# Kernel optimization log

Measured on AMD Instinct MI355X. Metric: run time of the kernel, lower is better.

## Reference

```python
import jax, jax.numpy as jnp
import numpy as np

N = 8192          # number of atoms
N_ELEM = 95       # r2r4 table size (elements 0..94)
EPS = 1e-12


def setup_inputs() -> dict:
    key = jax.random.key(0)
    k1, k2, k3 = jax.random.split(key, 3)
    atomic_numbers = jax.random.randint(k1, (N,), 0, N_ELEM)
    # positions in a ~60 Angstrom box so pair distances are realistic
    positions = jax.random.uniform(k2, (N, 3), dtype=jnp.float32) * 60.0
    r2r4 = jax.random.uniform(k3, (N_ELEM,), dtype=jnp.float32)
    # Becke-Johnson damping parameters (PBE D3-BJ)
    a1 = jnp.float32(0.4289)
    a2 = jnp.float32(4.4407)
    s6 = jnp.float32(1.0)
    s8 = jnp.float32(0.7875)
    return {"atomic_numbers": atomic_numbers, "positions": positions,
            "r2r4": r2r4, "a1": a1, "a2": a2, "s6": s6, "s8": s8}


def reference(atomic_numbers, positions, r2r4, a1, a2, s6, s8):
    # Per-atom-type gather (present in source; mathematically unused because
    # the source hard-codes c6 = c8 = 1 via all-ones LazyTensors).
    r2r4_z = r2r4[atomic_numbers]                      # (N,)

    # All-pairs squared distances. d appears only as d^6 and d^8, which are
    # polynomials in d2, so no sqrt is needed (also keeps diagonal smooth).
    diff = positions[:, None, :] - positions[None, :, :]   # (N, N, 3)
    d2 = jnp.sum(diff * diff, axis=-1)                     # (N, N)
    d6 = d2 * d2 * d2
    d8 = d6 * d2

    # c6 = c8 = 1  =>  tmp = a1 * sqrt(c8/c6) + a2 = a1 + a2
    tmp = a1 + a2
    tmp2 = tmp * tmp
    tmp6 = tmp2 * tmp2 * tmp2
    tmp8 = tmp6 * tmp2

    c6 = jnp.float32(1.0)
    c8 = jnp.float32(1.0)
    D_ij = -s6 * c6 / (d6 + tmp6 + EPS) - s8 * c8 / (d8 + tmp8 + EPS)

    # mask d > eps  <=>  d2 > eps^2 (removes self-terms)
    mask = d2 > EPS * EPS
    D_ij = jnp.where(mask, D_ij, jnp.float32(0.0))

    # a_i = sum_j D_ij ; energy = sum_i a_i
    return jnp.sum(D_ij) + jnp.float32(0.0) * jnp.sum(r2r4_z)
```

## Files before the change

kernel.cpp:

```cpp
#include <hip/hip_runtime.h>

#define NA 8192
#define TILE 128
#define NT (NA / TILE)
#define NBLK (NT * (NT + 1) / 2)
#define NSPLIT 4
#define BLOCK (TILE * NSPLIT)
#define JPT (TILE / NSPLIT)
#define NSLOT 16
#define S_OF(r) ((r) * NT - (r) * ((r) - 1) / 2)

__global__ __launch_bounds__(BLOCK, 8) void dftd3_pair_energy(
    const float* __restrict__ pos,
    const float* __restrict__ p_a1, const float* __restrict__ p_a2,
    const float* __restrict__ p_s6, const float* __restrict__ p_s8,
    float* __restrict__ partial)
{
    const int b = blockIdx.x;
    int ti = (int)((2 * NT + 1 - sqrtf((float)((2 * NT + 1) * (2 * NT + 1) - 8 * b))) * 0.5f);
    if (ti > NT - 1) ti = NT - 1;
    if (ti < 0) ti = 0;
    while (S_OF(ti + 1) <= b) ++ti;
    while (S_OF(ti) > b) --ti;
    const int tj = ti + (b - S_OF(ti));

    const int tid  = threadIdx.x;
    const int li   = tid & (TILE - 1);
    const int part = __builtin_amdgcn_readfirstlane(tid >> 7);

    const int i = ti * TILE + li;
    const float xi = pos[3 * i + 0];
    const float yi = pos[3 * i + 1];
    const float zi = pos[3 * i + 2];

    const float a1 = p_a1[0], a2 = p_a2[0];
    const float s6 = p_s6[0], s8 = p_s8[0];
    const float tmp  = a1 + a2;
    const float tmp2 = tmp * tmp;
    const float tmp6 = tmp2 * tmp2 * tmp2;
    const float tmp8 = tmp6 * tmp2;
    const float T6 = tmp6 + 1e-12f;
    const float T8 = tmp8 + 1e-12f;
    const float ns6 = -s6, ns8 = -s8;
    const float EPS2 = 1e-24f;

    const float* __restrict__ pj = pos + 3 * (tj * TILE + part * JPT);

    float acc0 = 0.0f, acc1 = 0.0f;

    auto body = [&](int k, bool masked) {
        float px = pj[3 * k + 0];
        float py = pj[3 * k + 1];
        float pz = pj[3 * k + 2];
        float dx = xi - px;
        float dy = yi - py;
        float dz = zi - pz;
        float d2 = fmaf(dx, dx, fmaf(dy, dy, dz * dz));
        float d4 = d2 * d2;
        float d6 = d4 * d2;
        float d8 = d4 * d4;
        float A  = d6 + T6;
        float B  = d8 + T8;
        float num = fmaf(ns6, B, ns8 * A);
        if (masked) num = (d2 > EPS2) ? num : 0.0f;
        float r = __builtin_amdgcn_rcpf(A * B);
        if (k & 1) acc1 = fmaf(num, r, acc1);
        else       acc0 = fmaf(num, r, acc0);
    };

    if (ti == tj) {
        #pragma unroll 8
        for (int k = 0; k < JPT; ++k) body(k, true);
    } else {
        #pragma unroll 8
        for (int k = 0; k < JPT; ++k) body(k, false);
    }

    float acc = acc0 + acc1;
    if (ti != tj) acc *= 2.0f;

    #pragma unroll
    for (int off = 32; off > 0; off >>= 1)
        acc += __shfl_xor(acc, off, 64);

    __shared__ float wsum[BLOCK / 64];
    if ((tid & 63) == 0) wsum[tid >> 6] = acc;
    __syncthreads();
    if (tid == 0) {
        float s = 0.0f;
        #pragma unroll
        for (int w = 0; w < BLOCK / 64; ++w) s += wsum[w];
        atomicAdd(&partial[b & (NSLOT - 1)], s);
    }
}

__global__ void reduce_slots(const float* __restrict__ partial, float* __restrict__ out)
{
    if (threadIdx.x == 0) {
        float s = 0.0f;
        #pragma unroll
        for (int k = 0; k < NSLOT; ++k) s += partial[k];
        out[0] = s;
    }
}

extern "C" void kernel_launch(void* const* d_in, const int* in_sizes, int n_in,
                              void* d_out, int out_size, void* d_ws, size_t ws_size,
                              hipStream_t stream) {
    const float* pos = (const float*)d_in[1];
    const float* a1  = (const float*)d_in[3];
    const float* a2  = (const float*)d_in[4];
    const float* s6  = (const float*)d_in[5];
    const float* s8  = (const float*)d_in[6];
    float* partial = (float*)d_ws;
    float* out = (float*)d_out;

    hipMemsetAsync(partial, 0, NSLOT * sizeof(float), stream);

    dftd3_pair_energy<<<dim3(NBLK), BLOCK, 0, stream>>>(pos, a1, a2, s6, s8, partial);
    reduce_slots<<<1, 64, 0, stream>>>(partial, out);
}
```

Baseline: 95.07 us.

## Assign 64x64 triangular tiles per wavefront and broadcast j positions via readlane

Each wavefront now owns a 64x64 tile of the upper-triangular pair matrix. Each lane loads one j position into a register, and the k-th position is broadcast to the whole wave with readlane instead of being re-read from global memory in the inner loop. This removes per-iteration global loads and gives finer triangular scheduling with 8 wave-jobs per block. The partial-sum slots grow to 64 and are spread apart by a stride to reduce atomic contention. There are more diagonal tiles with masked work, and NWJOB must divide evenly by 8 (8256/8=1032, so it does).

```diff
diff --git a/kernel.cpp b/kernel.cpp
--- a/kernel.cpp
+++ b/kernel.cpp
@@ -1,14 +1,19 @@
 #include <hip/hip_runtime.h>
 
 #define NA 8192
-#define TILE 128
-#define NT (NA / TILE)
-#define NBLK (NT * (NT + 1) / 2)
-#define NSPLIT 4
-#define BLOCK (TILE * NSPLIT)
-#define JPT (TILE / NSPLIT)
-#define NSLOT 16
-#define S_OF(r) ((r) * NT - (r) * ((r) - 1) / 2)
+#define WT 64
+#define NTW (NA / WT)
+#define NWJOB (NTW * (NTW + 1) / 2)
+#define WPB 8
+#define BLOCK (WPB * 64)
+#define NBLK (NWJOB / WPB)
+#define NSLOT 64
+#define SLOT_STRIDE 16
+#define S_OF(r) ((r) * NTW - (r) * ((r) - 1) / 2)
+
+__device__ __forceinline__ float bcast(float v, int k) {
+    return __int_as_float(__builtin_amdgcn_readlane(__float_as_int(v), k));
+}
 
 __global__ __launch_bounds__(BLOCK, 8) void dftd3_pair_energy(
     const float* __restrict__ pos,
@@ -16,22 +21,25 @@
     const float* __restrict__ p_s6, const float* __restrict__ p_s8,
     float* __restrict__ partial)
 {
-    const int b = blockIdx.x;
-    int ti = (int)((2 * NT + 1 - sqrtf((float)((2 * NT + 1) * (2 * NT + 1) - 8 * b))) * 0.5f);
-    if (ti > NT - 1) ti = NT - 1;
-    if (ti < 0) ti = 0;
-    while (S_OF(ti + 1) <= b) ++ti;
-    while (S_OF(ti) > b) --ti;
-    const int tj = ti + (b - S_OF(ti));
+    const int tid  = threadIdx.x;
+    const int lane = tid & 63;
+    const int w = __builtin_amdgcn_readfirstlane(blockIdx.x * WPB + (tid >> 6));
 
-    const int tid  = threadIdx.x;
-    const int li   = tid & (TILE - 1);
-    const int part = __builtin_amdgcn_readfirstlane(tid >> 7);
+    int wi = (int)((2 * NTW + 1 - sqrtf((float)((2 * NTW + 1) * (2 * NTW + 1) - 8 * w))) * 0.5f);
+    if (wi > NTW - 1) wi = NTW - 1;
+    if (wi < 0) wi = 0;
+    while (S_OF(wi + 1) <= w) ++wi;
+    while (S_OF(wi) > w) --wi;
+    const int wj = wi + (w - S_OF(wi));
 
-    const int i = ti * TILE + li;
+    const int i = wi * WT + lane;
     const float xi = pos[3 * i + 0];
     const float yi = pos[3 * i + 1];
     const float zi = pos[3 * i + 2];
+    const int j = wj * WT + lane;
+    const float vxj = pos[3 * j + 0];
+    const float vyj = pos[3 * j + 1];
+    const float vzj = pos[3 * j + 2];
 
     const float a1 = p_a1[0], a2 = p_a2[0];
     const float s6 = p_s6[0], s8 = p_s8[0];
@@ -44,17 +52,15 @@
     const float ns6 = -s6, ns8 = -s8;
     const float EPS2 = 1e-24f;
 
-    const float* __restrict__ pj = pos + 3 * (tj * TILE + part * JPT);
-
     float acc0 = 0.0f, acc1 = 0.0f;
 
     auto body = [&](int k, bool masked) {
-        float px = pj[3 * k + 0];
-        float py = pj[3 * k + 1];
-        float pz = pj[3 * k + 2];
-        float dx = xi - px;
-        float dy = yi - py;
-        float dz = zi - pz;
+        float sx = bcast(vxj, k);
+        float sy = bcast(vyj, k);
+        float sz = bcast(vzj, k);
+        float dx = xi - sx;
+        float dy = yi - sy;
+        float dz = zi - sz;
         float d2 = fmaf(dx, dx, fmaf(dy, dy, dz * dz));
         float d4 = d2 * d2;
         float d6 = d4 * d2;
@@ -68,29 +74,29 @@
         else       acc0 = fmaf(num, r, acc0);
     };
 
-    if (ti == tj) {
+    if (wi == wj) {
         #pragma unroll 8
-        for (int k = 0; k < JPT; ++k) body(k, true);
+        for (int k = 0; k < WT; ++k) body(k, true);
     } else {
         #pragma unroll 8
-        for (int k = 0; k < JPT; ++k) body(k, false);
+        for (int k = 0; k < WT; ++k) body(k, false);
     }
 
     float acc = acc0 + acc1;
-    if (ti != tj) acc *= 2.0f;
+    if (wi != wj) acc *= 2.0f;
 
     #pragma unroll
     for (int off = 32; off > 0; off >>= 1)
         acc += __shfl_xor(acc, off, 64);
 
-    __shared__ float wsum[BLOCK / 64];
-    if ((tid & 63) == 0) wsum[tid >> 6] = acc;
+    __shared__ float wsum[WPB];
+    if (lane == 0) wsum[tid >> 6] = acc;
     __syncthreads();
     if (tid == 0) {
         float s = 0.0f;
         #pragma unroll
-        for (int w = 0; w < BLOCK / 64; ++w) s += wsum[w];
-        atomicAdd(&partial[b & (NSLOT - 1)], s);
+        for (int q = 0; q < WPB; ++q) s += wsum[q];
+        atomicAdd(&partial[(blockIdx.x & (NSLOT - 1)) * SLOT_STRIDE], s);
     }
 }
 
@@ -99,7 +105,7 @@
     if (threadIdx.x == 0) {
         float s = 0.0f;
         #pragma unroll
-        for (int k = 0; k < NSLOT; ++k) s += partial[k];
+        for (int k = 0; k < NSLOT; ++k) s += partial[k * SLOT_STRIDE];
         out[0] = s;
     }
 }
@@ -115,7 +121,7 @@
     float* partial = (float*)d_ws;
     float* out = (float*)d_out;
 
-    hipMemsetAsync(partial, 0, NSLOT * sizeof(float), stream);
+    hipMemsetAsync(partial, 0, NSLOT * SLOT_STRIDE * sizeof(float), stream);
 
     dftd3_pair_energy<<<dim3(NBLK), BLOCK, 0, stream>>>(pos, a1, a2, s6, s8, partial);
     reduce_slots<<<1, 64, 0, stream>>>(partial, out);
```

Result: no change. 94.94 us (-0.1%).
